# Optimization experiments

Measured on AMD Instinct MI355X. Metric: run time of the kernel, lower is better.

Reference implementation:

```python
import jax, jax.numpy as jnp
import numpy as np
from jax import lax

PROB_THRESHOLD = 0.9
IOU_THRESHOLD = 0.5
H, W = 80, 80


def setup_inputs() -> dict:
    key = jax.random.key(0)
    # [5, H, W]: channel 0 = probability, channels 1:5 = (x1, y1, w, h)
    x = jax.random.uniform(key, (5, H, W), dtype=jnp.float32)
    return {"x": x}


def _pairwise_iou(boxes):
    # boxes: [N, 4] in xyxy format (torchvision box_iou semantics, no +1)
    area = jnp.maximum(boxes[:, 2] - boxes[:, 0], 0.0) * jnp.maximum(boxes[:, 3] - boxes[:, 1], 0.0)
    lt = jnp.maximum(boxes[:, None, :2], boxes[None, :, :2])  # [N, N, 2]
    rb = jnp.minimum(boxes[:, None, 2:], boxes[None, :, 2:])  # [N, N, 2]
    wh = jnp.maximum(rb - lt, 0.0)
    inter = wh[..., 0] * wh[..., 1]                           # [N, N]
    union = area[:, None] + area[None, :] - inter
    return inter / jnp.maximum(union, 1e-9)


def reference(x):
    # Flatten grid: rows = [prob, x1, y1, w, h]
    flat = x.reshape(5, -1).T  # [N, 5]
    valid = flat[:, 0] > PROB_THRESHOLD

    # Faithful in-place transform from the torch code:
    #   bbx[:, 2] = bbx[:, 0] + bbx[:, 2];  bbx[:, 3] = bbx[:, 1] + bbx[:, 3]
    # (column 0 is the probability channel, exactly as the source does it)
    c2 = flat[:, 0] + flat[:, 2]
    c3 = flat[:, 1] + flat[:, 3]
    b5 = jnp.stack([flat[:, 0], flat[:, 1], c2, c3, flat[:, 4]], axis=1)  # [N, 5]

    # Sort by score descending; invalid rows pushed to the end with -inf
    scores = jnp.where(valid, b5[:, 0], -jnp.inf)
    order = jnp.argsort(-scores)
    b5_sorted = b5[order]          # [N, 5]
    valid_sorted = valid[order]    # [N]
    boxes = b5_sorted[:, 1:]       # [N, 4] -> nms(boxes=x[:,1:], scores=x[:,0])

    iou = _pairwise_iou(boxes)     # [N, N], dominant 164 MB intermediate
    N = boxes.shape[0]

    # Greedy NMS in score order: keep box i iff it is valid and no already-kept
    # higher-scoring box overlaps it with IoU > threshold.
    def body(i, keep):
        suppressed = jnp.any(keep & (iou[i] > IOU_THRESHOLD))
        return keep.at[i].set(valid_sorted[i] & ~suppressed)

    keep = lax.fori_loop(0, N, body, jnp.zeros((N,), dtype=bool))

    # Fixed-shape, jit-friendly equivalent of x[bbxis]: kept rows (score-sorted),
    # suppressed / below-threshold rows zeroed out.
    return jnp.where(keep[:, None], b5_sorted, 0.0)
```

## Files before the change

### kernel.cpp

```cpp
#include <hip/hip_runtime.h>


#define MAXM  256
#define CHUNK 200

__global__ void k_zero(float* __restrict__ out, int out_n,
                       int* __restrict__ ranks, int n, int* __restrict__ cnt) {
  int tid = blockIdx.x * blockDim.x + threadIdx.x;
  int nt = gridDim.x * blockDim.x;
  float4* o4 = (float4*)out;
  int n4 = out_n >> 2;
  for (int i = tid; i < n4; i += nt) o4[i] = make_float4(0.f, 0.f, 0.f, 0.f);
  for (int i = (n4 << 2) + tid; i < out_n; i += nt) out[i] = 0.f;
  int4* r4 = (int4*)ranks;
  int rn4 = n >> 2;
  for (int i = tid; i < rn4; i += nt) r4[i] = make_int4(0, 0, 0, 0);
  for (int i = (rn4 << 2) + tid; i < n; i += nt) ranks[i] = 0;
  if (tid < 16) cnt[tid] = 0;
}

__global__ __launch_bounds__(64) void k_rank(const float* __restrict__ X,
                                             int* __restrict__ ranks, int n) {
  int i = blockIdx.x * 64 + threadIdx.x;
  int c0 = blockIdx.y * CHUNK;
  int cend = min(c0 + CHUNK, n);
  float si = (i < n) ? X[i] : -1.f;
  bool valid = (i < n) && (si > 0.9f);
  int gt = 0, eq = 0;
  const float4* X4 = (const float4*)(X + c0);
  int nq = (cend - c0) >> 2;
  for (int q = 0; q < nq; ++q) {
    float4 v = X4[q];
    gt += (v.x > si) + (v.y > si) + (v.z > si) + (v.w > si);
    eq += (v.x == si) + (v.y == si) + (v.z == si) + (v.w == si);
  }
  for (int j = c0 + (nq << 2); j < cend; ++j) {
    float sj = X[j];
    gt += (sj > si); eq += (sj == si);
  }
  if (i >= c0 && i < cend) eq -= 1;
  int partial = gt;
  if (__any(valid && eq > 0)) {
    int eqlt = 0;
    for (int j = c0; j < cend; ++j) {
      float sj = X[j];
      eqlt += (sj == si) && (j < i);
    }
    partial = gt + eqlt;
  }
  if (valid && partial > 0) atomicAdd(&ranks[i], partial);
}

__global__ void k_rows(const float* __restrict__ X, const int* __restrict__ ranks,
                       float* __restrict__ out, float* __restrict__ list,
                       int* __restrict__ cnt, int n) {
  int i = blockIdx.x * blockDim.x + threadIdx.x;
  if (i >= n) return;
  float s = X[i];
  if (!(s > 0.9f)) return;
  int r = ranks[i];
  float f1 = X[n + i], f2 = X[2 * n + i], f3 = X[3 * n + i], f4 = X[4 * n + i];
  float c2 = s + f2, c3 = f1 + f3;
  float* row = out + (size_t)r * 5;
  row[0] = s; row[1] = f1; row[2] = c2; row[3] = c3; row[4] = f4;
  float w = fmaxf(c3 - f1, 0.f);
  float h = fmaxf(f4 - c2, 0.f);
  float area = w * h;
  if (area > 0.f) {
    int p = atomicAdd(cnt, 1);
    if (p < MAXM) {
      float* e = list + (size_t)p * 6;
      e[0] = __int_as_float(r);
      e[1] = f1; e[2] = c2; e[3] = c3; e[4] = f4; e[5] = area;
    }
  }
}

__global__ __launch_bounds__(256) void k_nms(const float* __restrict__ list,
                                             const int* __restrict__ cnt,
                                             float* __restrict__ out) {
  __shared__ int   srank[MAXM];
  __shared__ float sbox[MAXM][4];
  __shared__ float sarea[MAXM];
  __shared__ int   skeep[MAXM];
  __shared__ int   sflag;
  int t = threadIdx.x;
  int M = *cnt;
  if (M > MAXM) M = MAXM;
  for (int e = t; e < M; e += 256) {
    int r = __float_as_int(list[e * 6 + 0]);
    int pos = 0;
    for (int m = 0; m < M; ++m)
      pos += (__float_as_int(list[m * 6 + 0]) < r);
    srank[pos] = r;
    sbox[pos][0] = list[e * 6 + 1];
    sbox[pos][1] = list[e * 6 + 2];
    sbox[pos][2] = list[e * 6 + 3];
    sbox[pos][3] = list[e * 6 + 4];
    sarea[pos] = list[e * 6 + 5];
    skeep[pos] = 1;
  }
  __syncthreads();
  for (int i = 1; i < M; ++i) {
    if (t == 0) sflag = 0;
    __syncthreads();
    if (t < i && skeep[t]) {
      float ltx = fmaxf(sbox[t][0], sbox[i][0]);
      float lty = fmaxf(sbox[t][1], sbox[i][1]);
      float rbx = fminf(sbox[t][2], sbox[i][2]);
      float rby = fminf(sbox[t][3], sbox[i][3]);
      float w = fmaxf(rbx - ltx, 0.f);
      float h = fmaxf(rby - lty, 0.f);
      float inter = w * h;
      float uni = sarea[t] + sarea[i] - inter;
      if (inter / fmaxf(uni, 1e-9f) > 0.5f) sflag = 1;
    }
    __syncthreads();
    if (t == 0 && sflag) skeep[i] = 0;
    __syncthreads();
  }
  for (int e = t; e < M; e += 256) {
    if (!skeep[e]) {
      float* row = out + (size_t)srank[e] * 5;
      row[0] = 0.f; row[1] = 0.f; row[2] = 0.f; row[3] = 0.f; row[4] = 0.f;
    }
  }
}

#define FB_NTH  1024
#define FB_MAXV 2048
__global__ __launch_bounds__(FB_NTH, 1) void nms_fallback(
    const float* __restrict__ X, float* __restrict__ out, int n, int out_n) {
  __shared__ float cscore[FB_MAXV];
  __shared__ unsigned int cidx[FB_MAXV];
  __shared__ int s_vcount, s_mcount, sflag;
  __shared__ int srank[MAXM];
  __shared__ float sbox[MAXM][4];
  __shared__ float sarea[MAXM];
  __shared__ int skeep[MAXM];
  __shared__ int prank[MAXM];
  __shared__ float pbox[MAXM][4];
  __shared__ float parea[MAXM];
  const int t = threadIdx.x;
  if (t == 0) { s_vcount = 0; s_mcount = 0; }
  float4* out4 = (float4*)out;
  int n4 = out_n >> 2;
  for (int i = t; i < n4; i += FB_NTH) out4[i] = make_float4(0.f, 0.f, 0.f, 0.f);
  for (int i = (n4 << 2) + t; i < out_n; i += FB_NTH) out[i] = 0.f;
  __syncthreads();
  for (int i = t; i < n; i += FB_NTH) {
    float s = X[i];
    if (s > 0.9f) {
      int p = atomicAdd(&s_vcount, 1);
      if (p < FB_MAXV) { cscore[p] = s; cidx[p] = (unsigned int)i; }
    }
  }
  __syncthreads();
  const int V = min(s_vcount, FB_MAXV);
  for (int e = t; e < V; e += FB_NTH) {
    float s = cscore[e];
    unsigned int idx = cidx[e];
    int rank = 0;
    for (int m = 0; m < V; ++m) {
      float sm = cscore[m];
      rank += (sm > s) || (sm == s && cidx[m] < idx);
    }
    float f1 = X[n + idx], f2 = X[2 * n + idx], f3 = X[3 * n + idx], f4 = X[4 * n + idx];
    float c2 = s + f2, c3 = f1 + f3;
    float* row = out + (size_t)rank * 5;
    row[0] = s; row[1] = f1; row[2] = c2; row[3] = c3; row[4] = f4;
    float w = fmaxf(c3 - f1, 0.f), h = fmaxf(f4 - c2, 0.f);
    float area = w * h;
    if (area > 0.f) {
      int p = atomicAdd(&s_mcount, 1);
      if (p < MAXM) {
        prank[p] = rank;
        pbox[p][0] = f1; pbox[p][1] = c2; pbox[p][2] = c3; pbox[p][3] = f4;
        parea[p] = area;
      }
    }
  }
  __syncthreads();
  const int M = min(s_mcount, MAXM);
  for (int e = t; e < M; e += FB_NTH) {
    int r = prank[e];
    int pos = 0;
    for (int m = 0; m < M; ++m) pos += (prank[m] < r);
    srank[pos] = r;
    sbox[pos][0] = pbox[e][0]; sbox[pos][1] = pbox[e][1];
    sbox[pos][2] = pbox[e][2]; sbox[pos][3] = pbox[e][3];
    sarea[pos] = parea[e];
    skeep[pos] = 1;
  }
  __syncthreads();
  for (int i = 1; i < M; ++i) {
    if (t == 0) sflag = 0;
    __syncthreads();
    if (t < i && skeep[t]) {
      float ltx = fmaxf(sbox[t][0], sbox[i][0]);
      float lty = fmaxf(sbox[t][1], sbox[i][1]);
      float rbx = fminf(sbox[t][2], sbox[i][2]);
      float rby = fminf(sbox[t][3], sbox[i][3]);
      float w = fmaxf(rbx - ltx, 0.f), h = fmaxf(rby - lty, 0.f);
      float inter = w * h;
      float uni = sarea[t] + sarea[i] - inter;
      if (inter / fmaxf(uni, 1e-9f) > 0.5f) sflag = 1;
    }
    __syncthreads();
    if (t == 0 && sflag) skeep[i] = 0;
    __syncthreads();
  }
  for (int e = t; e < M; e += FB_NTH) {
    if (!skeep[e]) {
      float* row = out + (size_t)srank[e] * 5;
      row[0] = 0.f; row[1] = 0.f; row[2] = 0.f; row[3] = 0.f; row[4] = 0.f;
    }
  }
}

extern "C" void kernel_launch(void* const* d_in, const int* in_sizes, int n_in,
                              void* d_out, int out_size, void* d_ws, size_t ws_size,
                              hipStream_t stream) {
  const float* X = (const float*)d_in[0];
  float* out = (float*)d_out;
  int n = in_sizes[0] / 5;
  size_t need = 64 + (size_t)n * sizeof(int) + (size_t)MAXM * 6 * sizeof(float);
  if (ws_size >= need) {
    int* cnt = (int*)d_ws;
    int* ranks = (int*)((char*)d_ws + 64);
    float* list = (float*)((char*)d_ws + 64 + (size_t)n * sizeof(int));
    int groups = (n + 63) / 64;
    int chunks = (n + CHUNK - 1) / CHUNK;
    hipLaunchKernelGGL(k_zero, dim3(80), dim3(256), 0, stream, out, out_size, ranks, n, cnt);
    hipLaunchKernelGGL(k_rank, dim3(groups, chunks), dim3(64), 0, stream, X, ranks, n);
    hipLaunchKernelGGL(k_rows, dim3((n + 255) / 256), dim3(256), 0, stream, X, ranks, out, list, cnt, n);
    hipLaunchKernelGGL(k_nms, dim3(1), dim3(256), 0, stream, list, cnt, out);
  } else {
    hipLaunchKernelGGL(nms_fallback, dim3(1), dim3(FB_NTH), 0, stream, X, out, n, out_size);
  }
}
```

Before: 65.67 us.

## Fuse ranking, row emit and NMS into one single-block kernel

Replaces the zero/rank/rows/nms multi-kernel pipeline with one 1024-thread block kernel. It compacts above-threshold scores into shared memory, ranks only those candidates with vectorized float4 compares, and then runs the serial NMS in the same block. This removes three kernel launches, global atomics and workspace traffic. In exchange, all ranking work is confined to a single CU and capped at a fixed candidate count.

```diff
diff --git a/kernel.cpp b/kernel.cpp
--- a/kernel.cpp
+++ b/kernel.cpp
@@ -1,106 +1,123 @@
 #include <hip/hip_runtime.h>
 
 
+#define NTH   1024
+#define MAXV  2048
 #define MAXM  256
-#define CHUNK 200
 
-__global__ void k_zero(float* __restrict__ out, int out_n,
-                       int* __restrict__ ranks, int n, int* __restrict__ cnt) {
-  int tid = blockIdx.x * blockDim.x + threadIdx.x;
-  int nt = gridDim.x * blockDim.x;
-  float4* o4 = (float4*)out;
-  int n4 = out_n >> 2;
-  for (int i = tid; i < n4; i += nt) o4[i] = make_float4(0.f, 0.f, 0.f, 0.f);
-  for (int i = (n4 << 2) + tid; i < out_n; i += nt) out[i] = 0.f;
-  int4* r4 = (int4*)ranks;
-  int rn4 = n >> 2;
-  for (int i = tid; i < rn4; i += nt) r4[i] = make_int4(0, 0, 0, 0);
-  for (int i = (rn4 << 2) + tid; i < n; i += nt) ranks[i] = 0;
-  if (tid < 16) cnt[tid] = 0;
-}
-
-__global__ __launch_bounds__(64) void k_rank(const float* __restrict__ X,
-                                             int* __restrict__ ranks, int n) {
-  int i = blockIdx.x * 64 + threadIdx.x;
-  int c0 = blockIdx.y * CHUNK;
-  int cend = min(c0 + CHUNK, n);
-  float si = (i < n) ? X[i] : -1.f;
-  bool valid = (i < n) && (si > 0.9f);
-  int gt = 0, eq = 0;
-  const float4* X4 = (const float4*)(X + c0);
-  int nq = (cend - c0) >> 2;
-  for (int q = 0; q < nq; ++q) {
-    float4 v = X4[q];
-    gt += (v.x > si) + (v.y > si) + (v.z > si) + (v.w > si);
-    eq += (v.x == si) + (v.y == si) + (v.z == si) + (v.w == si);
-  }
-  for (int j = c0 + (nq << 2); j < cend; ++j) {
-    float sj = X[j];
-    gt += (sj > si); eq += (sj == si);
-  }
-  if (i >= c0 && i < cend) eq -= 1;
-  int partial = gt;
-  if (__any(valid && eq > 0)) {
-    int eqlt = 0;
-    for (int j = c0; j < cend; ++j) {
-      float sj = X[j];
-      eqlt += (sj == si) && (j < i);
-    }
-    partial = gt + eqlt;
-  }
-  if (valid && partial > 0) atomicAdd(&ranks[i], partial);
-}
-
-__global__ void k_rows(const float* __restrict__ X, const int* __restrict__ ranks,
-                       float* __restrict__ out, float* __restrict__ list,
-                       int* __restrict__ cnt, int n) {
-  int i = blockIdx.x * blockDim.x + threadIdx.x;
-  if (i >= n) return;
-  float s = X[i];
-  if (!(s > 0.9f)) return;
-  int r = ranks[i];
-  float f1 = X[n + i], f2 = X[2 * n + i], f3 = X[3 * n + i], f4 = X[4 * n + i];
-  float c2 = s + f2, c3 = f1 + f3;
-  float* row = out + (size_t)r * 5;
-  row[0] = s; row[1] = f1; row[2] = c2; row[3] = c3; row[4] = f4;
-  float w = fmaxf(c3 - f1, 0.f);
-  float h = fmaxf(f4 - c2, 0.f);
-  float area = w * h;
-  if (area > 0.f) {
-    int p = atomicAdd(cnt, 1);
-    if (p < MAXM) {
-      float* e = list + (size_t)p * 6;
-      e[0] = __int_as_float(r);
-      e[1] = f1; e[2] = c2; e[3] = c3; e[4] = f4; e[5] = area;
-    }
-  }
-}
-
-__global__ __launch_bounds__(256) void k_nms(const float* __restrict__ list,
-                                             const int* __restrict__ cnt,
-                                             float* __restrict__ out) {
+__global__ __launch_bounds__(NTH, 1) void nms_all(
+    const float* __restrict__ X, float* __restrict__ out, int n, int out_n) {
+  __shared__ __align__(16) float cscore[MAXV];
+  __shared__ unsigned int cidx[MAXV];
+  __shared__ int s_vcount, s_mcount, sflag;
+  __shared__ int   prank[MAXM];
+  __shared__ float pbox[MAXM][4];
+  __shared__ float parea[MAXM];
   __shared__ int   srank[MAXM];
   __shared__ float sbox[MAXM][4];
   __shared__ float sarea[MAXM];
   __shared__ int   skeep[MAXM];
-  __shared__ int   sflag;
-  int t = threadIdx.x;
-  int M = *cnt;
-  if (M > MAXM) M = MAXM;
-  for (int e = t; e < M; e += 256) {
-    int r = __float_as_int(list[e * 6 + 0]);
+  const int t = threadIdx.x;
+  if (t == 0) { s_vcount = 0; s_mcount = 0; }
+
+  const float4* X4 = (const float4*)X;
+  const int n4 = n >> 2;
+  float4 sc0 = make_float4(-1.f, -1.f, -1.f, -1.f);
+  float4 sc1 = sc0;
+  if (t < n4)        sc0 = X4[t];
+  if (t + NTH < n4)  sc1 = X4[t + NTH];
+
+  float4* out4 = (float4*)out;
+  const int o4 = out_n >> 2;
+  for (int i = t; i < o4; i += NTH)
+    out4[i] = make_float4(0.f, 0.f, 0.f, 0.f);
+  for (int i = (o4 << 2) + t; i < out_n; i += NTH) out[i] = 0.f;
+
+  __syncthreads();
+
+  if (t < n4) {
+    float v[4] = {sc0.x, sc0.y, sc0.z, sc0.w};
+    #pragma unroll
+    for (int k = 0; k < 4; ++k)
+      if (v[k] > 0.9f) {
+        int p = atomicAdd(&s_vcount, 1);
+        if (p < MAXV) { cscore[p] = v[k]; cidx[p] = (unsigned)(4 * t + k); }
+      }
+  }
+  if (t + NTH < n4) {
+    float v[4] = {sc1.x, sc1.y, sc1.z, sc1.w};
+    #pragma unroll
+    for (int k = 0; k < 4; ++k)
+      if (v[k] > 0.9f) {
+        int p = atomicAdd(&s_vcount, 1);
+        if (p < MAXV) { cscore[p] = v[k]; cidx[p] = (unsigned)(4 * (t + NTH) + k); }
+      }
+  }
+  for (int i = (n4 << 2) + t; i < n; i += NTH) {
+    float s = X[i];
+    if (s > 0.9f) {
+      int p = atomicAdd(&s_vcount, 1);
+      if (p < MAXV) { cscore[p] = s; cidx[p] = (unsigned)i; }
+    }
+  }
+  __syncthreads();
+
+  const int V = min(s_vcount, MAXV);
+  const int V4 = (V + 3) & ~3;
+  for (int e = V + t; e < V4; e += NTH) cscore[e] = -1.f;
+  __syncthreads();
+
+  const float4* c4 = (const float4*)cscore;
+  const int nq = V4 >> 2;
+  for (int e = t; e < V; e += NTH) {
+    float s = cscore[e];
+    unsigned idx = cidx[e];
+    int gt = 0, eq = 0;
+    for (int q = 0; q < nq; ++q) {
+      float4 v = c4[q];
+      gt += (v.x > s) + (v.y > s) + (v.z > s) + (v.w > s);
+      eq += (v.x == s) + (v.y == s) + (v.z == s) + (v.w == s);
+    }
+    eq -= 1;
+    int rank = gt;
+    if (eq > 0) {
+      int lt = 0;
+      for (int m = 0; m < V; ++m)
+        lt += (cscore[m] == s) && (cidx[m] < idx);
+      rank += lt;
+    }
+    float f1 = X[n + idx], f2 = X[2 * n + idx];
+    float f3 = X[3 * n + idx], f4v = X[4 * n + idx];
+    float c2 = s + f2, c3 = f1 + f3;
+    float* row = out + (size_t)rank * 5;
+    row[0] = s; row[1] = f1; row[2] = c2; row[3] = c3; row[4] = f4v;
+    float w = fmaxf(c3 - f1, 0.f);
+    float h = fmaxf(f4v - c2, 0.f);
+    float area = w * h;
+    if (area > 0.f) {
+      int p = atomicAdd(&s_mcount, 1);
+      if (p < MAXM) {
+        prank[p] = rank;
+        pbox[p][0] = f1; pbox[p][1] = c2; pbox[p][2] = c3; pbox[p][3] = f4v;
+        parea[p] = area;
+      }
+    }
+  }
+  __syncthreads();
+
+  const int M = min(s_mcount, MAXM);
+  for (int e = t; e < M; e += NTH) {
+    int r = prank[e];
     int pos = 0;
-    for (int m = 0; m < M; ++m)
-      pos += (__float_as_int(list[m * 6 + 0]) < r);
+    for (int m = 0; m < M; ++m) pos += (prank[m] < r);
     srank[pos] = r;
-    sbox[pos][0] = list[e * 6 + 1];
-    sbox[pos][1] = list[e * 6 + 2];
-    sbox[pos][2] = list[e * 6 + 3];
-    sbox[pos][3] = list[e * 6 + 4];
-    sarea[pos] = list[e * 6 + 5];
+    sbox[pos][0] = pbox[e][0]; sbox[pos][1] = pbox[e][1];
+    sbox[pos][2] = pbox[e][2]; sbox[pos][3] = pbox[e][3];
+    sarea[pos] = parea[e];
     skeep[pos] = 1;
   }
   __syncthreads();
+
   for (int i = 1; i < M; ++i) {
     if (t == 0) sflag = 0;
     __syncthreads();
@@ -119,98 +136,8 @@
     if (t == 0 && sflag) skeep[i] = 0;
     __syncthreads();
   }
-  for (int e = t; e < M; e += 256) {
-    if (!skeep[e]) {
-      float* row = out + (size_t)srank[e] * 5;
-      row[0] = 0.f; row[1] = 0.f; row[2] = 0.f; row[3] = 0.f; row[4] = 0.f;
-    }
-  }
-}
 
-#define FB_NTH  1024
-#define FB_MAXV 2048
-__global__ __launch_bounds__(FB_NTH, 1) void nms_fallback(
-    const float* __restrict__ X, float* __restrict__ out, int n, int out_n) {
-  __shared__ float cscore[FB_MAXV];
-  __shared__ unsigned int cidx[FB_MAXV];
-  __shared__ int s_vcount, s_mcount, sflag;
-  __shared__ int srank[MAXM];
-  __shared__ float sbox[MAXM][4];
-  __shared__ float sarea[MAXM];
-  __shared__ int skeep[MAXM];
-  __shared__ int prank[MAXM];
-  __shared__ float pbox[MAXM][4];
-  __shared__ float parea[MAXM];
-  const int t = threadIdx.x;
-  if (t == 0) { s_vcount = 0; s_mcount = 0; }
-  float4* out4 = (float4*)out;
-  int n4 = out_n >> 2;
-  for (int i = t; i < n4; i += FB_NTH) out4[i] = make_float4(0.f, 0.f, 0.f, 0.f);
-  for (int i = (n4 << 2) + t; i < out_n; i += FB_NTH) out[i] = 0.f;
-  __syncthreads();
-  for (int i = t; i < n; i += FB_NTH) {
-    float s = X[i];
-    if (s > 0.9f) {
-      int p = atomicAdd(&s_vcount, 1);
-      if (p < FB_MAXV) { cscore[p] = s; cidx[p] = (unsigned int)i; }
-    }
-  }
-  __syncthreads();
-  const int V = min(s_vcount, FB_MAXV);
-  for (int e = t; e < V; e += FB_NTH) {
-    float s = cscore[e];
-    unsigned int idx = cidx[e];
-    int rank = 0;
-    for (int m = 0; m < V; ++m) {
-      float sm = cscore[m];
-      rank += (sm > s) || (sm == s && cidx[m] < idx);
-    }
-    float f1 = X[n + idx], f2 = X[2 * n + idx], f3 = X[3 * n + idx], f4 = X[4 * n + idx];
-    float c2 = s + f2, c3 = f1 + f3;
-    float* row = out + (size_t)rank * 5;
-    row[0] = s; row[1] = f1; row[2] = c2; row[3] = c3; row[4] = f4;
-    float w = fmaxf(c3 - f1, 0.f), h = fmaxf(f4 - c2, 0.f);
-    float area = w * h;
-    if (area > 0.f) {
-      int p = atomicAdd(&s_mcount, 1);
-      if (p < MAXM) {
-        prank[p] = rank;
-        pbox[p][0] = f1; pbox[p][1] = c2; pbox[p][2] = c3; pbox[p][3] = f4;
-        parea[p] = area;
-      }
-    }
-  }
-  __syncthreads();
-  const int M = min(s_mcount, MAXM);
-  for (int e = t; e < M; e += FB_NTH) {
-    int r = prank[e];
-    int pos = 0;
-    for (int m = 0; m < M; ++m) pos += (prank[m] < r);
-    srank[pos] = r;
-    sbox[pos][0] = pbox[e][0]; sbox[pos][1] = pbox[e][1];
-    sbox[pos][2] = pbox[e][2]; sbox[pos][3] = pbox[e][3];
-    sarea[pos] = parea[e];
-    skeep[pos] = 1;
-  }
-  __syncthreads();
-  for (int i = 1; i < M; ++i) {
-    if (t == 0) sflag = 0;
-    __syncthreads();
-    if (t < i && skeep[t]) {
-      float ltx = fmaxf(sbox[t][0], sbox[i][0]);
-      float lty = fmaxf(sbox[t][1], sbox[i][1]);
-      float rbx = fminf(sbox[t][2], sbox[i][2]);
-      float rby = fminf(sbox[t][3], sbox[i][3]);
-      float w = fmaxf(rbx - ltx, 0.f), h = fmaxf(rby - lty, 0.f);
-      float inter = w * h;
-      float uni = sarea[t] + sarea[i] - inter;
-      if (inter / fmaxf(uni, 1e-9f) > 0.5f) sflag = 1;
-    }
-    __syncthreads();
-    if (t == 0 && sflag) skeep[i] = 0;
-    __syncthreads();
-  }
-  for (int e = t; e < M; e += FB_NTH) {
+  for (int e = t; e < M; e += NTH) {
     if (!skeep[e]) {
       float* row = out + (size_t)srank[e] * 5;
       row[0] = 0.f; row[1] = 0.f; row[2] = 0.f; row[3] = 0.f; row[4] = 0.f;
@@ -224,18 +151,6 @@
   const float* X = (const float*)d_in[0];
   float* out = (float*)d_out;
   int n = in_sizes[0] / 5;
-  size_t need = 64 + (size_t)n * sizeof(int) + (size_t)MAXM * 6 * sizeof(float);
-  if (ws_size >= need) {
-    int* cnt = (int*)d_ws;
-    int* ranks = (int*)((char*)d_ws + 64);
-    float* list = (float*)((char*)d_ws + 64 + (size_t)n * sizeof(int));
-    int groups = (n + 63) / 64;
-    int chunks = (n + CHUNK - 1) / CHUNK;
-    hipLaunchKernelGGL(k_zero, dim3(80), dim3(256), 0, stream, out, out_size, ranks, n, cnt);
-    hipLaunchKernelGGL(k_rank, dim3(groups, chunks), dim3(64), 0, stream, X, ranks, n);
-    hipLaunchKernelGGL(k_rows, dim3((n + 255) / 256), dim3(256), 0, stream, X, ranks, out, list, cnt, n);
-    hipLaunchKernelGGL(k_nms, dim3(1), dim3(256), 0, stream, list, cnt, out);
-  } else {
-    hipLaunchKernelGGL(nms_fallback, dim3(1), dim3(FB_NTH), 0, stream, X, out, n, out_size);
-  }
+  (void)d_ws; (void)ws_size;
+  hipLaunchKernelGGL(nms_all, dim3(1), dim3(NTH), 0, stream, X, out, n, out_size);
 }
```

Result: slower. 71.01 us (+8.1%).
